# Kernel tuning notes

Hardware: AMD Instinct MI355X
Metric: run time of the kernel (lower is better)

Reference implementation:

```python
import jax, jax.numpy as jnp
import numpy as np

N_NODES = 20000
N_EDGES = 320000
D_IN = 256
D_HID = 256
D_OUT = 128
N_LAYERS = 5
BN_EPS = 1e-5
W_SCALE = 1.0 / np.sqrt(D_HID)


def setup_inputs() -> dict:
    key = jax.random.key(0)
    ks = jax.random.split(key, 16)
    x = jax.random.normal(ks[0], (N_NODES, D_IN), dtype=jnp.float32)
    edge_index = jax.random.randint(ks[1], (2, N_EDGES), 0, N_NODES, dtype=jnp.int32)
    W1 = jax.random.normal(ks[2], (N_LAYERS, D_IN, D_HID), dtype=jnp.float32) * W_SCALE
    b1 = jax.random.normal(ks[3], (N_LAYERS, D_HID), dtype=jnp.float32) * 0.01
    W2a = jax.random.normal(ks[4], (N_LAYERS - 1, D_HID, D_HID), dtype=jnp.float32) * W_SCALE
    b2a = jax.random.normal(ks[5], (N_LAYERS - 1, D_HID), dtype=jnp.float32) * 0.01
    W2_last = jax.random.normal(ks[6], (D_HID, D_OUT), dtype=jnp.float32) * W_SCALE
    b2_last = jax.random.normal(ks[7], (D_OUT,), dtype=jnp.float32) * 0.01
    eps = jnp.zeros((N_LAYERS,), dtype=jnp.float32)
    bn_gamma = jnp.ones((N_LAYERS - 1, D_HID), dtype=jnp.float32)
    bn_beta = jnp.zeros((N_LAYERS - 1, D_HID), dtype=jnp.float32)
    bn_mean = jax.random.normal(ks[8], (N_LAYERS - 1, D_HID), dtype=jnp.float32) * 0.1
    bn_var = jax.random.uniform(ks[9], (N_LAYERS - 1, D_HID), dtype=jnp.float32, minval=0.5, maxval=1.5)
    return {"x": x, "edge_index": edge_index, "W1": W1, "b1": b1, "W2a": W2a,
            "b2a": b2a, "W2_last": W2_last, "b2_last": b2_last, "eps": eps,
            "bn_gamma": bn_gamma, "bn_beta": bn_beta, "bn_mean": bn_mean, "bn_var": bn_var}


def reference(x, edge_index, W1, b1, W2a, b2a, W2_last, b2_last, eps,
              bn_gamma, bn_beta, bn_mean, bn_var):
    src, dst = edge_index[0], edge_index[1]
    n = x.shape[0]

    def gin_conv(h, e, w1, bb1, w2, bb2):
        # scatter-add neighbor sum: agg[v] = sum_{(u->v)} h[u]
        agg = jax.ops.segment_sum(h[src], dst, num_segments=n)  # [N, d]
        z = (1.0 + e) * h + agg
        z = jax.nn.relu(z @ w1 + bb1)
        return z @ w2 + bb2

    h = x
    for i in range(N_LAYERS - 1):
        h = gin_conv(h, eps[i], W1[i], b1[i], W2a[i], b2a[i])
        # BatchNorm1d in eval mode (running stats); dropout inactive at inference
        h = (h - bn_mean[i]) * jax.lax.rsqrt(bn_var[i] + BN_EPS) * bn_gamma[i] + bn_beta[i]
        h = jax.nn.relu(h)
    out = gin_conv(h, eps[N_LAYERS - 1], W1[N_LAYERS - 1], b1[N_LAYERS - 1], W2_last, b2_last)
    return out
```

## Files before the change

kernel.cpp:

```cpp
#include <hip/hip_runtime.h>
#include <stdint.h>

#define NN    20000
#define NE    320000
#define MPAD  20096
#define DD    256
#define DOUT  128
#define CAP   64
#define RS    40
#define SS    1288
#define STS   264
#define SFS   132

typedef unsigned short u16;
typedef __attribute__((ext_vector_type(8))) __bf16 bf16x8;
typedef __attribute__((ext_vector_type(4))) float  f32x4;

__device__ __forceinline__ uint32_t f2b(float f){
  union { float f; uint32_t u; } x; x.f = f;
  uint32_t r = x.u + 0x7FFFu + ((x.u >> 16) & 1u);
  return r >> 16;
}
__device__ __forceinline__ float blo(uint32_t p){ union{uint32_t u;float f;}x; x.u=p<<16;         return x.f; }
__device__ __forceinline__ float bhi(uint32_t p){ union{uint32_t u;float f;}x; x.u=p&0xFFFF0000u; return x.f; }
__device__ __forceinline__ int   fiu(float f){ union{float f;int i;}x; x.f=f; return x.i; }
__device__ __forceinline__ float uif(int i){ union{int i;float f;}x; x.i=i; return x.f; }

#define TB 152
#define XB (MPAD/4)
#define EB ((NE+255)/256)
__global__ __launch_bounds__(256) void prep_all(
    const float* __restrict__ x, const int* __restrict__ src, const int* __restrict__ dst,
    const float* __restrict__ W1, const float* __restrict__ W2a, const float* __restrict__ W2l,
    u16* __restrict__ W1t, u16* __restrict__ W2at, u16* __restrict__ W2lt,
    u16* __restrict__ h0, int* __restrict__ cnt, int* __restrict__ csr)
{
  __shared__ u16 Ts[64][65];
  int b = blockIdx.x, tid = threadIdx.x;
  if (b < TB){
    const float* srcp; u16* dstp; int ldS, k0, n0;
    if (b < 80){
      int layer = b >> 4, sub = b & 15;
      srcp = W1 + layer*65536; dstp = W1t + layer*65536; ldS = 256;
      k0 = (sub >> 2)*64; n0 = (sub & 3)*64;
    } else if (b < 144){
      int bb = b - 80; int layer = bb >> 4, sub = bb & 15;
      srcp = W2a + layer*65536; dstp = W2at + layer*65536; ldS = 256;
      k0 = (sub >> 2)*64; n0 = (sub & 3)*64;
    } else {
      int sub = b - 144;
      srcp = W2l; dstp = W2lt; ldS = 128;
      k0 = (sub >> 1)*64; n0 = (sub & 1)*64;
    }
    int c = tid & 63, r0 = tid >> 6;
    #pragma unroll
    for (int i = 0; i < 16; ++i){
      int r = r0 + i*4;
      Ts[r][c] = (u16)f2b(srcp[(size_t)(k0 + r)*ldS + n0 + c]);
    }
    __syncthreads();
    #pragma unroll
    for (int i = 0; i < 16; ++i){
      int n = r0 + i*4;
      dstp[(size_t)(n0 + n)*256 + k0 + c] = Ts[c][n];
    }
  } else if (b < TB + XB){
    int bb = b - TB;
    int row  = bb*4 + (tid >> 6);
    int lane = tid & 63;
    uint2 o = make_uint2(0u, 0u);
    if (row < NN){
      float4 f = *(const float4*)(x + (size_t)row*DD + lane*4);
      o.x = f2b(f.x) | (f2b(f.y) << 16);
      o.y = f2b(f.z) | (f2b(f.w) << 16);
    }
    *(uint2*)(h0 + (size_t)row*DD + lane*4) = o;
  } else {
    int e = (b - TB - XB)*256 + tid;
    if (e < NE){
      int d = dst[e];
      int slot = atomicAdd(&cnt[d], 1);
      if (slot < CAP) csr[d*CAP + slot] = src[e];
    }
  }
}

__global__ __launch_bounds__(256, 3) void gin_fused(
    const u16* __restrict__ hin, const int* __restrict__ cnt, const int* __restrict__ csr,
    const float* __restrict__ eps_arr, int layer,
    const u16* __restrict__ w1, const float* __restrict__ b1,
    const u16* __restrict__ w2, const float* __restrict__ b2,
    const float* __restrict__ gma, const float* __restrict__ bta,
    const float* __restrict__ mu,  const float* __restrict__ var,
    u16* __restrict__ hout, float* __restrict__ outf, int last)
{
  __shared__ __align__(16) u16 As[8*SS];
  int tid  = threadIdx.x;
  int lane = tid & 63, w = tid >> 6;
  int m0 = blockIdx.x * 32;
  int l15 = lane & 15, l4 = lane >> 4;

  {
    float e = 1.0f + eps_arr[layer];
    int half = lane >> 5, kl = lane & 31;
    int xi = (lane ^ 32) << 2;
    const u16* hrow = hin + kl*8;
    u16* dstL = As + (kl >> 2)*SS + (kl & 3)*8;
    for (int i = 0; i < 8; ++i){
      int row = w*8 + i;
      int v = __builtin_amdgcn_readfirstlane(m0 + row);
      float a0=0.f,a1=0.f,a2=0.f,a3=0.f,a4=0.f,a5=0.f,a6=0.f,a7=0.f;
      if (v < NN){
        uint4 ov = *(const uint4*)(hrow + (size_t)v*DD);
        int deg = cnt[v]; deg = deg > CAP ? CAP : deg;
        const int* lst = csr + (size_t)v*CAP;
        for (int base = 0; base < deg; base += 16){
          int4 q[4];
          #pragma unroll
          for (int c = 0; c < 4; ++c) q[c] = *(const int4*)(lst + base + 4*c);
          int idv[8];
          #pragma unroll
          for (int c = 0; c < 4; ++c){
            idv[2*c]   = half ? q[c].y : q[c].x;
            idv[2*c+1] = half ? q[c].w : q[c].z;
          }
          uint4 rv[8];
          #pragma unroll
          for (int c = 0; c < 8; ++c){
            int g = (base + 2*c + half < deg) ? idv[c] : v;
            rv[c] = *(const uint4*)(hrow + (size_t)g*DD);
          }
          #pragma unroll
          for (int c = 0; c < 8; ++c){
            if (base + 2*c + half < deg){
              a0 += blo(rv[c].x); a1 += bhi(rv[c].x);
              a2 += blo(rv[c].y); a3 += bhi(rv[c].y);
              a4 += blo(rv[c].z); a5 += bhi(rv[c].z);
              a6 += blo(rv[c].w); a7 += bhi(rv[c].w);
            }
          }
        }
        float eh = half ? 0.0f : e;
        a0 += eh*blo(ov.x); a1 += eh*bhi(ov.x);
        a2 += eh*blo(ov.y); a3 += eh*bhi(ov.y);
        a4 += eh*blo(ov.z); a5 += eh*bhi(ov.z);
        a6 += eh*blo(ov.w); a7 += eh*bhi(ov.w);
      }
      a0 += uif(__builtin_amdgcn_ds_bpermute(xi, fiu(a0)));
      a1 += uif(__builtin_amdgcn_ds_bpermute(xi, fiu(a1)));
      a2 += uif(__builtin_amdgcn_ds_bpermute(xi, fiu(a2)));
      a3 += uif(__builtin_amdgcn_ds_bpermute(xi, fiu(a3)));
      a4 += uif(__builtin_amdgcn_ds_bpermute(xi, fiu(a4)));
      a5 += uif(__builtin_amdgcn_ds_bpermute(xi, fiu(a5)));
      a6 += uif(__builtin_amdgcn_ds_bpermute(xi, fiu(a6)));
      a7 += uif(__builtin_amdgcn_ds_bpermute(xi, fiu(a7)));
      if (half == 0){
        uint4 o;
        o.x = f2b(a0) | (f2b(a1) << 16);
        o.y = f2b(a2) | (f2b(a3) << 16);
        o.z = f2b(a4) | (f2b(a5) << 16);
        o.w = f2b(a6) | (f2b(a7) << 16);
        *(uint4*)(dstL + row*RS) = o;
      }
    }
  }
  __syncthreads();

  f32x4 acc1[4][2];
  #pragma unroll
  for (int i=0;i<4;++i)
    #pragma unroll
    for (int j=0;j<2;++j){ f32x4 zr={0.f,0.f,0.f,0.f}; acc1[i][j]=zr; }
  {
    int hidb = w*64;
    for (int s = 0; s < 8; ++s){
      bf16x8 af[4], bz[2];
      #pragma unroll
      for (int mi=0;mi<4;++mi)
        af[mi] = *(const bf16x8*)(w1 + (size_t)(hidb + mi*16 + l15)*DD + s*32 + l4*8);
      #pragma unroll
      for (int nj=0;nj<2;++nj)
        bz[nj] = *(const bf16x8*)(As + s*SS + (nj*16 + l15)*RS + l4*8);
      #pragma unroll
      for (int mi=0;mi<4;++mi)
        #pragma unroll
        for (int nj=0;nj<2;++nj)
          acc1[mi][nj] = __builtin_amdgcn_mfma_f32_16x16x32_bf16(af[mi], bz[nj], acc1[mi][nj], 0,0,0);
    }
  }
  __syncthreads();

  {
    int hidb = w*64;
    #pragma unroll
    for (int mi=0;mi<4;++mi){
      float4 bv = *(const float4*)(b1 + hidb + mi*16 + l4*4);
      int s2 = w*2 + (mi >> 1);
      int kp = (mi & 1)*16 + l4*4;
      #pragma unroll
      for (int nj=0;nj<2;++nj){
        int zrow = nj*16 + l15;
        float v0 = acc1[mi][nj][0] + bv.x; v0 = v0 > 0.f ? v0 : 0.f;
        float v1 = acc1[mi][nj][1] + bv.y; v1 = v1 > 0.f ? v1 : 0.f;
        float v2 = acc1[mi][nj][2] + bv.z; v2 = v2 > 0.f ? v2 : 0.f;
        float v3 = acc1[mi][nj][3] + bv.w; v3 = v3 > 0.f ? v3 : 0.f;
        uint2 pk;
        pk.x = f2b(v0) | (f2b(v1) << 16);
        pk.y = f2b(v2) | (f2b(v3) << 16);
        *(uint2*)(As + s2*SS + zrow*RS + kp) = pk;
      }
    }
  }
  __syncthreads();

  if (!last){
    f32x4 acc2[2][4];
    #pragma unroll
    for (int i=0;i<2;++i)
      #pragma unroll
      for (int j=0;j<4;++j){ f32x4 zr={0.f,0.f,0.f,0.f}; acc2[i][j]=zr; }
    int cb = w*64;
    for (int s = 0; s < 8; ++s){
      bf16x8 at[2], bw[4];
      #pragma unroll
      for (int i=0;i<2;++i)
        at[i] = *(const bf16x8*)(As + s*SS + (i*16 + l15)*RS + l4*8);
      #pragma unroll
      for (int j=0;j<4;++j)
        bw[j] = *(const bf16x8*)(w2 + (size_t)(cb + j*16 + l15)*DD + s*32 + l4*8);
      #pragma unroll
      for (int i=0;i<2;++i)
        #pragma unroll
        for (int j=0;j<4;++j)
          acc2[i][j] = __builtin_amdgcn_mfma_f32_16x16x32_bf16(at[i], bw[j], acc2[i][j], 0,0,0);
    }
    __syncthreads();
    u16* St = As;
    #pragma unroll
    for (int j=0;j<4;++j){
      int col = cb + j*16 + l15;
      float sc = rsqrtf(var[col] + 1e-5f) * gma[col];
      float sh = (b2[col] - mu[col]) * sc + bta[col];
      #pragma unroll
      for (int i=0;i<2;++i){
        #pragma unroll
        for (int r=0;r<4;++r){
          int row = i*16 + l4*4 + r;
          float vv = acc2[i][j][r]*sc + sh;
          vv = vv > 0.f ? vv : 0.f;
          St[row*STS + col] = (u16)f2b(vv);
        }
      }
    }
    __syncthreads();
    #pragma unroll
    for (int it = 0; it < 4; ++it){
      int idx = it*256 + tid;
      int row = idx >> 5, c = idx & 31;
      *(uint4*)(hout + (size_t)(m0 + row)*DD + c*8) = *(const uint4*)(St + row*STS + c*8);
    }
  } else {
    f32x4 acc2[2][2];
    #pragma unroll
    for (int i=0;i<2;++i)
      #pragma unroll
      for (int j=0;j<2;++j){ f32x4 zr={0.f,0.f,0.f,0.f}; acc2[i][j]=zr; }
    int cbk = w*32;
    for (int s = 0; s < 8; ++s){
      bf16x8 at[2], bw[2];
      #pragma unroll
      for (int i=0;i<2;++i)
        at[i] = *(const bf16x8*)(As + s*SS + (i*16 + l15)*RS + l4*8);
      #pragma unroll
      for (int j=0;j<2;++j)
        bw[j] = *(const bf16x8*)(w2 + (size_t)(cbk + j*16 + l15)*DD + s*32 + l4*8);
      #pragma unroll
      for (int i=0;i<2;++i)
        #pragma unroll
        for (int j=0;j<2;++j)
          acc2[i][j] = __builtin_amdgcn_mfma_f32_16x16x32_bf16(at[i], bw[j], acc2[i][j], 0,0,0);
    }
    __syncthreads();
    float* Sf = (float*)As;
    #pragma unroll
    for (int j=0;j<2;++j){
      int col = cbk + j*16 + l15;
      float sh = b2[col];
      #pragma unroll
      for (int i=0;i<2;++i){
        #pragma unroll
        for (int r=0;r<4;++r){
          int row = i*16 + l4*4 + r;
          Sf[row*SFS + col] = acc2[i][j][r] + sh;
        }
      }
    }
    __syncthreads();
    #pragma unroll
    for (int it = 0; it < 4; ++it){
      int idx = it*256 + tid;
      int row = idx >> 5, c = idx & 31;
      if (m0 + row < NN)
        *(uint4*)(outf + (size_t)(m0 + row)*DOUT + c*4) = *(const uint4*)(Sf + row*SFS + c*4);
    }
  }
}

extern "C" void kernel_launch(void* const* d_in, const int* in_sizes, int n_in,
                              void* d_out, int out_size, void* d_ws, size_t ws_size,
                              hipStream_t stream)
{
  const float* x     = (const float*)d_in[0];
  const int*   ei    = (const int*)  d_in[1];
  const float* W1    = (const float*)d_in[2];
  const float* b1    = (const float*)d_in[3];
  const float* W2a   = (const float*)d_in[4];
  const float* b2a   = (const float*)d_in[5];
  const float* W2l   = (const float*)d_in[6];
  const float* b2l   = (const float*)d_in[7];
  const float* eps   = (const float*)d_in[8];
  const float* gma   = (const float*)d_in[9];
  const float* bta   = (const float*)d_in[10];
  const float* mu    = (const float*)d_in[11];
  const float* var   = (const float*)d_in[12];
  float* out = (float*)d_out;

  char* ws = (char*)d_ws;
  size_t off = 0;
  auto alloc = [&](size_t bytes)->void*{
    void* p = ws + off; off += (bytes + 255) & ~(size_t)255; return p;
  };
  u16* h0   = (u16*)alloc((size_t)MPAD*DD*2);
  u16* h1   = (u16*)alloc((size_t)MPAD*DD*2);
  int* cnt  = (int*)alloc((size_t)NN*4);
  int* csr  = (int*)alloc((size_t)NN*CAP*4 + 64);
  u16* W1t  = (u16*)alloc((size_t)5*65536*2);
  u16* W2at = (u16*)alloc((size_t)4*65536*2);
  u16* W2lt = (u16*)alloc((size_t)32768*2);

  const int* srcA = ei;
  const int* dstA = ei + NE;

  hipMemsetAsync(cnt, 0, (size_t)NN*4, stream);
  prep_all<<<TB + XB + EB, 256, 0, stream>>>(x, srcA, dstA, W1, W2a, W2l,
                                             W1t, W2at, W2lt, h0, cnt, csr);

  u16* hbuf[2] = { h0, h1 };
  for (int L = 0; L < 5; ++L){
    const u16* hin = hbuf[L & 1];
    u16*       ho  = hbuf[1 - (L & 1)];
    if (L < 4){
      gin_fused<<<MPAD/32, 256, 0, stream>>>(hin, cnt, csr, eps, L,
          W1t + (size_t)L*65536, b1 + L*256,
          W2at + (size_t)L*65536, b2a + L*256,
          gma + L*256, bta + L*256, mu + L*256, var + L*256,
          ho, nullptr, 0);
    } else {
      gin_fused<<<MPAD/32, 256, 0, stream>>>(hin, cnt, csr, eps, L,
          W1t + (size_t)L*65536, b1 + L*256,
          W2lt, b2l,
          nullptr, nullptr, nullptr, nullptr,
          nullptr, out, 1);
    }
  }
}
```

Baseline: 329.0 us.

## Split neighbor gather into a separate high-occupancy kernel before the MLP GEMM

Unfuses the per-layer kernel into a gather kernel (one wave per node, launch bounds allowing 8 blocks per CU) that writes the aggregated z to global memory, followed by a GEMM kernel that loads z into LDS. The goal is to give the latency-bound random gather more occupancy than the register-heavy fused GEMM kernel permits. The cost is an extra round trip of z through global memory and twice as many launches per layer. The grid is now NN/32, which divides evenly, so the padded rows are no longer processed.

```diff
diff --git a/kernel.cpp b/kernel.cpp
--- a/kernel.cpp
+++ b/kernel.cpp
@@ -74,7 +74,8 @@
       o.x = f2b(f.x) | (f2b(f.y) << 16);
       o.y = f2b(f.z) | (f2b(f.w) << 16);
     }
-    *(uint2*)(h0 + (size_t)row*DD + lane*4) = o;
+    if (row < MPAD)
+      *(uint2*)(h0 + (size_t)row*DD + lane*4) = o;
   } else {
     int e = (b - TB - XB)*256 + tid;
     if (e < NE){
@@ -85,9 +86,73 @@
   }
 }
 
-__global__ __launch_bounds__(256, 3) void gin_fused(
+__global__ __launch_bounds__(256, 8) void gather_z(
     const u16* __restrict__ hin, const int* __restrict__ cnt, const int* __restrict__ csr,
-    const float* __restrict__ eps_arr, int layer,
+    const float* __restrict__ eps_arr, int layer, u16* __restrict__ z)
+{
+  int lane = threadIdx.x & 63;
+  int v = __builtin_amdgcn_readfirstlane(blockIdx.x*4 + (threadIdx.x >> 6));
+  if (v >= NN) return;
+  float e = 1.0f + eps_arr[layer];
+  int half = lane >> 5, kl = lane & 31;
+  int xi = (lane ^ 32) << 2;
+  const u16* hrow = hin + kl*8;
+
+  float a0=0.f,a1=0.f,a2=0.f,a3=0.f,a4=0.f,a5=0.f,a6=0.f,a7=0.f;
+  uint4 ov = *(const uint4*)(hrow + (size_t)v*DD);
+  int deg = cnt[v]; deg = deg > CAP ? CAP : deg;
+  const int* lst = csr + (size_t)v*CAP;
+  for (int base = 0; base < deg; base += 16){
+    int4 q[4];
+    #pragma unroll
+    for (int c = 0; c < 4; ++c) q[c] = *(const int4*)(lst + base + 4*c);
+    int idv[8];
+    #pragma unroll
+    for (int c = 0; c < 4; ++c){
+      idv[2*c]   = half ? q[c].y : q[c].x;
+      idv[2*c+1] = half ? q[c].w : q[c].z;
+    }
+    uint4 rv[8];
+    #pragma unroll
+    for (int c = 0; c < 8; ++c){
+      int g = (base + 2*c + half < deg) ? idv[c] : v;
+      rv[c] = *(const uint4*)(hrow + (size_t)g*DD);
+    }
+    #pragma unroll
+    for (int c = 0; c < 8; ++c){
+      if (base + 2*c + half < deg){
+        a0 += blo(rv[c].x); a1 += bhi(rv[c].x);
+        a2 += blo(rv[c].y); a3 += bhi(rv[c].y);
+        a4 += blo(rv[c].z); a5 += bhi(rv[c].z);
+        a6 += blo(rv[c].w); a7 += bhi(rv[c].w);
+      }
+    }
+  }
+  float eh = half ? 0.0f : e;
+  a0 += eh*blo(ov.x); a1 += eh*bhi(ov.x);
+  a2 += eh*blo(ov.y); a3 += eh*bhi(ov.y);
+  a4 += eh*blo(ov.z); a5 += eh*bhi(ov.z);
+  a6 += eh*blo(ov.w); a7 += eh*bhi(ov.w);
+  a0 += uif(__builtin_amdgcn_ds_bpermute(xi, fiu(a0)));
+  a1 += uif(__builtin_amdgcn_ds_bpermute(xi, fiu(a1)));
+  a2 += uif(__builtin_amdgcn_ds_bpermute(xi, fiu(a2)));
+  a3 += uif(__builtin_amdgcn_ds_bpermute(xi, fiu(a3)));
+  a4 += uif(__builtin_amdgcn_ds_bpermute(xi, fiu(a4)));
+  a5 += uif(__builtin_amdgcn_ds_bpermute(xi, fiu(a5)));
+  a6 += uif(__builtin_amdgcn_ds_bpermute(xi, fiu(a6)));
+  a7 += uif(__builtin_amdgcn_ds_bpermute(xi, fiu(a7)));
+  if (half == 0){
+    uint4 o;
+    o.x = f2b(a0) | (f2b(a1) << 16);
+    o.y = f2b(a2) | (f2b(a3) << 16);
+    o.z = f2b(a4) | (f2b(a5) << 16);
+    o.w = f2b(a6) | (f2b(a7) << 16);
+    *(uint4*)(z + (size_t)v*DD + kl*8) = o;
+  }
+}
+
+__global__ __launch_bounds__(256, 3) void gin_mm(
+    const u16* __restrict__ zin,
     const u16* __restrict__ w1, const float* __restrict__ b1,
     const u16* __restrict__ w2, const float* __restrict__ b2,
     const float* __restrict__ gma, const float* __restrict__ bta,
@@ -100,69 +165,12 @@
   int m0 = blockIdx.x * 32;
   int l15 = lane & 15, l4 = lane >> 4;
 
-  {
-    float e = 1.0f + eps_arr[layer];
-    int half = lane >> 5, kl = lane & 31;
-    int xi = (lane ^ 32) << 2;
-    const u16* hrow = hin + kl*8;
-    u16* dstL = As + (kl >> 2)*SS + (kl & 3)*8;
-    for (int i = 0; i < 8; ++i){
-      int row = w*8 + i;
-      int v = __builtin_amdgcn_readfirstlane(m0 + row);
-      float a0=0.f,a1=0.f,a2=0.f,a3=0.f,a4=0.f,a5=0.f,a6=0.f,a7=0.f;
-      if (v < NN){
-        uint4 ov = *(const uint4*)(hrow + (size_t)v*DD);
-        int deg = cnt[v]; deg = deg > CAP ? CAP : deg;
-        const int* lst = csr + (size_t)v*CAP;
-        for (int base = 0; base < deg; base += 16){
-          int4 q[4];
-          #pragma unroll
-          for (int c = 0; c < 4; ++c) q[c] = *(const int4*)(lst + base + 4*c);
-          int idv[8];
-          #pragma unroll
-          for (int c = 0; c < 4; ++c){
-            idv[2*c]   = half ? q[c].y : q[c].x;
-            idv[2*c+1] = half ? q[c].w : q[c].z;
-          }
-          uint4 rv[8];
-          #pragma unroll
-          for (int c = 0; c < 8; ++c){
-            int g = (base + 2*c + half < deg) ? idv[c] : v;
-            rv[c] = *(const uint4*)(hrow + (size_t)g*DD);
-          }
-          #pragma unroll
-          for (int c = 0; c < 8; ++c){
-            if (base + 2*c + half < deg){
-              a0 += blo(rv[c].x); a1 += bhi(rv[c].x);
-              a2 += blo(rv[c].y); a3 += bhi(rv[c].y);
-              a4 += blo(rv[c].z); a5 += bhi(rv[c].z);
-              a6 += blo(rv[c].w); a7 += bhi(rv[c].w);
-            }
-          }
-        }
-        float eh = half ? 0.0f : e;
-        a0 += eh*blo(ov.x); a1 += eh*bhi(ov.x);
-        a2 += eh*blo(ov.y); a3 += eh*bhi(ov.y);
-        a4 += eh*blo(ov.z); a5 += eh*bhi(ov.z);
-        a6 += eh*blo(ov.w); a7 += eh*bhi(ov.w);
-      }
-      a0 += uif(__builtin_amdgcn_ds_bpermute(xi, fiu(a0)));
-      a1 += uif(__builtin_amdgcn_ds_bpermute(xi, fiu(a1)));
-      a2 += uif(__builtin_amdgcn_ds_bpermute(xi, fiu(a2)));
-      a3 += uif(__builtin_amdgcn_ds_bpermute(xi, fiu(a3)));
-      a4 += uif(__builtin_amdgcn_ds_bpermute(xi, fiu(a4)));
-      a5 += uif(__builtin_amdgcn_ds_bpermute(xi, fiu(a5)));
-      a6 += uif(__builtin_amdgcn_ds_bpermute(xi, fiu(a6)));
-      a7 += uif(__builtin_amdgcn_ds_bpermute(xi, fiu(a7)));
-      if (half == 0){
-        uint4 o;
-        o.x = f2b(a0) | (f2b(a1) << 16);
-        o.y = f2b(a2) | (f2b(a3) << 16);
-        o.z = f2b(a4) | (f2b(a5) << 16);
-        o.w = f2b(a6) | (f2b(a7) << 16);
-        *(uint4*)(dstL + row*RS) = o;
-      }
-    }
+  #pragma unroll
+  for (int it = 0; it < 4; ++it){
+    int idx = it*256 + tid;
+    int row = idx >> 5, kl = idx & 31;
+    uint4 zv = *(const uint4*)(zin + (size_t)(m0 + row)*DD + kl*8);
+    *(uint4*)(As + (kl >> 2)*SS + row*RS + (kl & 3)*8) = zv;
   }
   __syncthreads();
 
@@ -330,8 +338,8 @@
   auto alloc = [&](size_t bytes)->void*{
     void* p = ws + off; off += (bytes + 255) & ~(size_t)255; return p;
   };
-  u16* h0   = (u16*)alloc((size_t)MPAD*DD*2);
-  u16* h1   = (u16*)alloc((size_t)MPAD*DD*2);
+  u16* h    = (u16*)alloc((size_t)MPAD*DD*2);
+  u16* z    = (u16*)alloc((size_t)MPAD*DD*2);
   int* cnt  = (int*)alloc((size_t)NN*4);
   int* csr  = (int*)alloc((size_t)NN*CAP*4 + 64);
   u16* W1t  = (u16*)alloc((size_t)5*65536*2);
@@ -343,21 +351,19 @@
 
   hipMemsetAsync(cnt, 0, (size_t)NN*4, stream);
   prep_all<<<TB + XB + EB, 256, 0, stream>>>(x, srcA, dstA, W1, W2a, W2l,
-                                             W1t, W2at, W2lt, h0, cnt, csr);
-
-  u16* hbuf[2] = { h0, h1 };
+                                             W1t, W2at, W2lt, h, cnt, csr);
+
   for (int L = 0; L < 5; ++L){
-    const u16* hin = hbuf[L & 1];
-    u16*       ho  = hbuf[1 - (L & 1)];
+    gather_z<<<NN/4, 256, 0, stream>>>(h, cnt, csr, eps, L, z);
     if (L < 4){
-      gin_fused<<<MPAD/32, 256, 0, stream>>>(hin, cnt, csr, eps, L,
+      gin_mm<<<NN/32, 256, 0, stream>>>(z,
           W1t + (size_t)L*65536, b1 + L*256,
           W2at + (size_t)L*65536, b2a + L*256,
           gma + L*256, bta + L*256, mu + L*256, var + L*256,
-          ho, nullptr, 0);
+          h, nullptr, 0);
     } else {
-      gin_fused<<<MPAD/32, 256, 0, stream>>>(hin, cnt, csr, eps, L,
-          W1t + (size_t)L*65536, b1 + L*256,
+      gin_mm<<<NN/32, 256, 0, stream>>>(z,
+          W1t + (size_t)4*65536, b1 + 4*256,
           W2lt, b2l,
           nullptr, nullptr, nullptr, nullptr,
           nullptr, out, 1);
```

New measurement: 361.1 us. 9.7% more time.

## Store node features as per-row int8 with scales to shrink neighbor gather traffic

Applied to the files above, without the earlier changes.

Intermediate node features are stored as int8 with a per-row float scale instead of bf16, halving the bytes read in the random neighbor gather, which dominates each layer. The gather is reworked so 16-lane groups each handle one neighbor per step and are reduced with two cross-lane permutes. The layer epilogue quantizes its output rows, and the grid shrinks to 625 blocks, dropping padded rows. The exchange is added quantization error on the input features and on every hidden layer.

```diff
diff --git a/kernel.cpp b/kernel.cpp
--- a/kernel.cpp
+++ b/kernel.cpp
@@ -4,6 +4,7 @@
 #define NN    20000
 #define NE    320000
 #define MPAD  20096
+#define NBLK  625
 #define DD    256
 #define DOUT  128
 #define CAP   64
@@ -13,6 +14,7 @@
 #define SFS   132
 
 typedef unsigned short u16;
+typedef unsigned char  u8;
 typedef __attribute__((ext_vector_type(8))) __bf16 bf16x8;
 typedef __attribute__((ext_vector_type(4))) float  f32x4;
 
@@ -26,6 +28,13 @@
 __device__ __forceinline__ int   fiu(float f){ union{float f;int i;}x; x.f=f; return x.i; }
 __device__ __forceinline__ float uif(int i){ union{int i;float f;}x; x.i=i; return x.f; }
 
+__device__ __forceinline__ void acc4(float* a, uint32_t dw, float s){
+  a[0] += s * (float)(int)(int8_t)(dw);
+  a[1] += s * (float)(int)(int8_t)(dw >> 8);
+  a[2] += s * (float)(int)(int8_t)(dw >> 16);
+  a[3] += s * (float)(int)(int8_t)(dw >> 24);
+}
+
 #define TB 152
 #define XB (MPAD/4)
 #define EB ((NE+255)/256)
@@ -33,7 +42,7 @@
     const float* __restrict__ x, const int* __restrict__ src, const int* __restrict__ dst,
     const float* __restrict__ W1, const float* __restrict__ W2a, const float* __restrict__ W2l,
     u16* __restrict__ W1t, u16* __restrict__ W2at, u16* __restrict__ W2lt,
-    u16* __restrict__ h0, int* __restrict__ cnt, int* __restrict__ csr)
+    u8* __restrict__ hq0, float* __restrict__ hs0, int* __restrict__ cnt, int* __restrict__ csr)
 {
   __shared__ u16 Ts[64][65];
   int b = blockIdx.x, tid = threadIdx.x;
@@ -68,13 +77,21 @@
     int bb = b - TB;
     int row  = bb*4 + (tid >> 6);
     int lane = tid & 63;
-    uint2 o = make_uint2(0u, 0u);
-    if (row < NN){
-      float4 f = *(const float4*)(x + (size_t)row*DD + lane*4);
-      o.x = f2b(f.x) | (f2b(f.y) << 16);
-      o.y = f2b(f.z) | (f2b(f.w) << 16);
-    }
-    *(uint2*)(h0 + (size_t)row*DD + lane*4) = o;
+    float4 f = make_float4(0.f,0.f,0.f,0.f);
+    if (row < NN) f = *(const float4*)(x + (size_t)row*DD + lane*4);
+    float mx = fmaxf(fmaxf(fabsf(f.x), fabsf(f.y)), fmaxf(fabsf(f.z), fabsf(f.w)));
+    #pragma unroll
+    for (int m = 1; m < 64; m <<= 1) mx = fmaxf(mx, __shfl_xor(mx, m, 64));
+    float inv = mx > 0.f ? 127.0f/mx : 0.f;
+    uint32_t pk = 0;
+    pk |= (uint32_t)(u8)(int8_t)__float2int_rn(f.x*inv);
+    pk |= (uint32_t)(u8)(int8_t)__float2int_rn(f.y*inv) << 8;
+    pk |= (uint32_t)(u8)(int8_t)__float2int_rn(f.z*inv) << 16;
+    pk |= (uint32_t)(u8)(int8_t)__float2int_rn(f.w*inv) << 24;
+    if (row < MPAD){
+      *(uint32_t*)(hq0 + (size_t)row*DD + lane*4) = pk;
+      if (lane == 0) hs0[row] = mx * (1.0f/127.0f);
+    }
   } else {
     int e = (b - TB - XB)*256 + tid;
     if (e < NE){
@@ -86,13 +103,15 @@
 }
 
 __global__ __launch_bounds__(256, 3) void gin_fused(
-    const u16* __restrict__ hin, const int* __restrict__ cnt, const int* __restrict__ csr,
+    const u8* __restrict__ hq, const float* __restrict__ hs,
+    const int* __restrict__ cnt, const int* __restrict__ csr,
     const float* __restrict__ eps_arr, int layer,
     const u16* __restrict__ w1, const float* __restrict__ b1,
     const u16* __restrict__ w2, const float* __restrict__ b2,
     const float* __restrict__ gma, const float* __restrict__ bta,
     const float* __restrict__ mu,  const float* __restrict__ var,
-    u16* __restrict__ hout, float* __restrict__ outf, int last)
+    u8* __restrict__ hqo, float* __restrict__ hso,
+    float* __restrict__ outf, int last)
 {
   __shared__ __align__(16) u16 As[8*SS];
   int tid  = threadIdx.x;
@@ -102,65 +121,66 @@
 
   {
     float e = 1.0f + eps_arr[layer];
-    int half = lane >> 5, kl = lane & 31;
-    int xi = (lane ^ 32) << 2;
-    const u16* hrow = hin + kl*8;
-    u16* dstL = As + (kl >> 2)*SS + (kl & 3)*8;
+    int q2 = lane >> 4, kl = lane & 15;
+    int x16 = (lane ^ 16) << 2;
+    int x32 = (lane ^ 32) << 2;
+    const u8* hrow = hq + kl*16;
     for (int i = 0; i < 8; ++i){
       int row = w*8 + i;
       int v = __builtin_amdgcn_readfirstlane(m0 + row);
-      float a0=0.f,a1=0.f,a2=0.f,a3=0.f,a4=0.f,a5=0.f,a6=0.f,a7=0.f;
-      if (v < NN){
+      float a[16];
+      #pragma unroll
+      for (int j = 0; j < 16; ++j) a[j] = 0.f;
+      int deg = cnt[v]; deg = deg > CAP ? CAP : deg;
+      const int* lst = csr + (size_t)v*CAP;
+      for (int base = 0; base < deg; base += 16){
+        int4 qv[4];
+        #pragma unroll
+        for (int c = 0; c < 4; ++c) qv[c] = *(const int4*)(lst + base + 4*c);
+        uint4 rv[4]; float sv[4];
+        #pragma unroll
+        for (int c = 0; c < 4; ++c){
+          int slot = base + 4*c + q2;
+          int eidx = q2 == 0 ? qv[c].x : q2 == 1 ? qv[c].y : q2 == 2 ? qv[c].z : qv[c].w;
+          int g = slot < deg ? eidx : v;
+          rv[c] = *(const uint4*)(hrow + (size_t)g*DD);
+          float s = hs[g];
+          sv[c] = slot < deg ? s : 0.f;
+        }
+        #pragma unroll
+        for (int c = 0; c < 4; ++c){
+          acc4(a +  0, rv[c].x, sv[c]);
+          acc4(a +  4, rv[c].y, sv[c]);
+          acc4(a +  8, rv[c].z, sv[c]);
+          acc4(a + 12, rv[c].w, sv[c]);
+        }
+      }
+      {
         uint4 ov = *(const uint4*)(hrow + (size_t)v*DD);
-        int deg = cnt[v]; deg = deg > CAP ? CAP : deg;
-        const int* lst = csr + (size_t)v*CAP;
-        for (int base = 0; base < deg; base += 16){
-          int4 q[4];
-          #pragma unroll
-          for (int c = 0; c < 4; ++c) q[c] = *(const int4*)(lst + base + 4*c);
-          int idv[8];
-          #pragma unroll
-          for (int c = 0; c < 4; ++c){
-            idv[2*c]   = half ? q[c].y : q[c].x;
-            idv[2*c+1] = half ? q[c].w : q[c].z;
-          }
-          uint4 rv[8];
-          #pragma unroll
-          for (int c = 0; c < 8; ++c){
-            int g = (base + 2*c + half < deg) ? idv[c] : v;
-            rv[c] = *(const uint4*)(hrow + (size_t)g*DD);
-          }
-          #pragma unroll
-          for (int c = 0; c < 8; ++c){
-            if (base + 2*c + half < deg){
-              a0 += blo(rv[c].x); a1 += bhi(rv[c].x);
-              a2 += blo(rv[c].y); a3 += bhi(rv[c].y);
-              a4 += blo(rv[c].z); a5 += bhi(rv[c].z);
-              a6 += blo(rv[c].w); a7 += bhi(rv[c].w);
-            }
-          }
-        }
-        float eh = half ? 0.0f : e;
-        a0 += eh*blo(ov.x); a1 += eh*bhi(ov.x);
-        a2 += eh*blo(ov.y); a3 += eh*bhi(ov.y);
-        a4 += eh*blo(ov.z); a5 += eh*bhi(ov.z);
-        a6 += eh*blo(ov.w); a7 += eh*bhi(ov.w);
-      }
-      a0 += uif(__builtin_amdgcn_ds_bpermute(xi, fiu(a0)));
-      a1 += uif(__builtin_amdgcn_ds_bpermute(xi, fiu(a1)));
-      a2 += uif(__builtin_amdgcn_ds_bpermute(xi, fiu(a2)));
-      a3 += uif(__builtin_amdgcn_ds_bpermute(xi, fiu(a3)));
-      a4 += uif(__builtin_amdgcn_ds_bpermute(xi, fiu(a4)));
-      a5 += uif(__builtin_amdgcn_ds_bpermute(xi, fiu(a5)));
-      a6 += uif(__builtin_amdgcn_ds_bpermute(xi, fiu(a6)));
-      a7 += uif(__builtin_amdgcn_ds_bpermute(xi, fiu(a7)));
-      if (half == 0){
-        uint4 o;
-        o.x = f2b(a0) | (f2b(a1) << 16);
-        o.y = f2b(a2) | (f2b(a3) << 16);
-        o.z = f2b(a4) | (f2b(a5) << 16);
-        o.w = f2b(a6) | (f2b(a7) << 16);
-        *(uint4*)(dstL + row*RS) = o;
+        float se = (q2 == 0) ? e * hs[v] : 0.f;
+        acc4(a +  0, ov.x, se);
+        acc4(a +  4, ov.y, se);
+        acc4(a +  8, ov.z, se);
+        acc4(a + 12, ov.w, se);
+      }
+      #pragma unroll
+      for (int j = 0; j < 16; ++j){
+        a[j] += uif(__builtin_amdgcn_ds_bpermute(x16, fiu(a[j])));
+        a[j] += uif(__builtin_amdgcn_ds_bpermute(x32, fiu(a[j])));
+      }
+      if (q2 == 0){
+        uint4 o1, o2;
+        o1.x = f2b(a[0])  | (f2b(a[1])  << 16);
+        o1.y = f2b(a[2])  | (f2b(a[3])  << 16);
+        o1.z = f2b(a[4])  | (f2b(a[5])  << 16);
+        o1.w = f2b(a[6])  | (f2b(a[7])  << 16);
+        o2.x = f2b(a[8])  | (f2b(a[9])  << 16);
+        o2.y = f2b(a[10]) | (f2b(a[11]) << 16);
+        o2.z = f2b(a[12]) | (f2b(a[13]) << 16);
+        o2.w = f2b(a[14]) | (f2b(a[15]) << 16);
+        u16* dstL = As + (kl >> 1)*SS + row*RS + (kl & 1)*16;
+        *(uint4*)(dstL)     = o1;
+        *(uint4*)(dstL + 8) = o2;
       }
     }
   }
@@ -257,7 +277,24 @@
     for (int it = 0; it < 4; ++it){
       int idx = it*256 + tid;
       int row = idx >> 5, c = idx & 31;
-      *(uint4*)(hout + (size_t)(m0 + row)*DD + c*8) = *(const uint4*)(St + row*STS + c*8);
+      uint4 pk = *(const uint4*)(St + row*STS + c*8);
+      float f0 = blo(pk.x), f1 = bhi(pk.x), f2 = blo(pk.y), f3 = bhi(pk.y);
+      float f4 = blo(pk.z), f5 = bhi(pk.z), f6 = blo(pk.w), f7 = bhi(pk.w);
+      float mx = fmaxf(fmaxf(fmaxf(f0,f1), fmaxf(f2,f3)), fmaxf(fmaxf(f4,f5), fmaxf(f6,f7)));
+      #pragma unroll
+      for (int m = 1; m < 32; m <<= 1) mx = fmaxf(mx, __shfl_xor(mx, m, 64));
+      float inv = mx > 0.f ? 127.0f/mx : 0.f;
+      uint32_t b0 = 0, b1v = 0;
+      b0  |= (uint32_t)(u8)(int8_t)__float2int_rn(f0*inv);
+      b0  |= (uint32_t)(u8)(int8_t)__float2int_rn(f1*inv) << 8;
+      b0  |= (uint32_t)(u8)(int8_t)__float2int_rn(f2*inv) << 16;
+      b0  |= (uint32_t)(u8)(int8_t)__float2int_rn(f3*inv) << 24;
+      b1v |= (uint32_t)(u8)(int8_t)__float2int_rn(f4*inv);
+      b1v |= (uint32_t)(u8)(int8_t)__float2int_rn(f5*inv) << 8;
+      b1v |= (uint32_t)(u8)(int8_t)__float2int_rn(f6*inv) << 16;
+      b1v |= (uint32_t)(u8)(int8_t)__float2int_rn(f7*inv) << 24;
+      *(uint2*)(hqo + (size_t)(m0 + row)*DD + c*8) = make_uint2(b0, b1v);
+      if (c == 0) hso[m0 + row] = mx * (1.0f/127.0f);
     }
   } else {
     f32x4 acc2[2][2];
@@ -300,8 +337,7 @@
     for (int it = 0; it < 4; ++it){
       int idx = it*256 + tid;
       int row = idx >> 5, c = idx & 31;
-      if (m0 + row < NN)
-        *(uint4*)(outf + (size_t)(m0 + row)*DOUT + c*4) = *(const uint4*)(Sf + row*SFS + c*4);
+      *(uint4*)(outf + (size_t)(m0 + row)*DOUT + c*4) = *(const uint4*)(Sf + row*SFS + c*4);
     }
   }
 }
@@ -330,37 +366,42 @@
   auto alloc = [&](size_t bytes)->void*{
     void* p = ws + off; off += (bytes + 255) & ~(size_t)255; return p;
   };
-  u16* h0   = (u16*)alloc((size_t)MPAD*DD*2);
-  u16* h1   = (u16*)alloc((size_t)MPAD*DD*2);
-  int* cnt  = (int*)alloc((size_t)NN*4);
-  int* csr  = (int*)alloc((size_t)NN*CAP*4 + 64);
-  u16* W1t  = (u16*)alloc((size_t)5*65536*2);
-  u16* W2at = (u16*)alloc((size_t)4*65536*2);
-  u16* W2lt = (u16*)alloc((size_t)32768*2);
+  u8*    hq0 = (u8*)   alloc((size_t)MPAD*DD);
+  u8*    hq1 = (u8*)   alloc((size_t)MPAD*DD);
+  float* hs0 = (float*)alloc((size_t)MPAD*4);
+  float* hs1 = (float*)alloc((size_t)MPAD*4);
+  int*   cnt = (int*)  alloc((size_t)NN*4);
+  int*   csr = (int*)  alloc((size_t)NN*CAP*4 + 64);
+  u16*  W1t  = (u16*)  alloc((size_t)5*65536*2);
+  u16*  W2at = (u16*)  alloc((size_t)4*65536*2);
+  u16*  W2lt = (u16*)  alloc((size_t)32768*2);
 
   const int* srcA = ei;
   const int* dstA = ei + NE;
 
   hipMemsetAsync(cnt, 0, (size_t)NN*4, stream);
   prep_all<<<TB + XB + EB, 256, 0, stream>>>(x, srcA, dstA, W1, W2a, W2l,
-                                             W1t, W2at, W2lt, h0, cnt, csr);
-
-  u16* hbuf[2] = { h0, h1 };
+                                             W1t, W2at, W2lt, hq0, hs0, cnt, csr);
+
+  u8*    hq[2] = { hq0, hq1 };
+  float* hsv[2] = { hs0, hs1 };
   for (int L = 0; L < 5; ++L){
-    const u16* hin = hbuf[L & 1];
-    u16*       ho  = hbuf[1 - (L & 1)];
+    const u8*    hin = hq[L & 1];
+    const float* hsi = hsv[L & 1];
+    u8*    ho  = hq[1 - (L & 1)];
+    float* hso = hsv[1 - (L & 1)];
     if (L < 4){
-      gin_fused<<<MPAD/32, 256, 0, stream>>>(hin, cnt, csr, eps, L,
+      gin_fused<<<NBLK, 256, 0, stream>>>(hin, hsi, cnt, csr, eps, L,
           W1t + (size_t)L*65536, b1 + L*256,
           W2at + (size_t)L*65536, b2a + L*256,
           gma + L*256, bta + L*256, mu + L*256, var + L*256,
-          ho, nullptr, 0);
+          ho, hso, nullptr, 0);
     } else {
-      gin_fused<<<MPAD/32, 256, 0, stream>>>(hin, cnt, csr, eps, L,
-          W1t + (size_t)L*65536, b1 + L*256,
+      gin_fused<<<NBLK, 256, 0, stream>>>(hin, hsi, cnt, csr, eps, L,
+          W1t + (size_t)4*65536, b1 + 4*256,
           W2lt, b2l,
           nullptr, nullptr, nullptr, nullptr,
-          nullptr, out, 1);
+          nullptr, nullptr, out, 1);
     }
   }
 }
```

Measured after the change: 352.2 us. 1.07x slower.

## Merge five per-layer launches into one persistent kernel with grid barriers

Applied to the files above, without the earlier changes.

Replaces the five per-layer gin_fused launches with a single gin_all kernel that loops over layers and synchronises all 628 blocks through an atomic-counter grid barrier between layers. The aim is to remove kernel launch gaps and tail effects between layers. It relies on all 628 blocks being co-resident (256 CUs at 3 blocks per CU allows it) and adds spin-wait barrier cost plus a memset of the counter. A bounds guard on h0 writes in prep is also added.

```diff
diff --git a/kernel.cpp b/kernel.cpp
--- a/kernel.cpp
+++ b/kernel.cpp
@@ -4,6 +4,7 @@
 #define NN    20000
 #define NE    320000
 #define MPAD  20096
+#define NBLK  628
 #define DD    256
 #define DOUT  128
 #define CAP   64
@@ -25,6 +26,17 @@
 __device__ __forceinline__ float bhi(uint32_t p){ union{uint32_t u;float f;}x; x.u=p&0xFFFF0000u; return x.f; }
 __device__ __forceinline__ int   fiu(float f){ union{float f;int i;}x; x.f=f; return x.i; }
 __device__ __forceinline__ float uif(int i){ union{int i;float f;}x; x.i=i; return x.f; }
+
+__device__ __forceinline__ void grid_barrier(int* bar, int target){
+  __syncthreads();
+  if (threadIdx.x == 0){
+    __threadfence();
+    __hip_atomic_fetch_add(bar, 1, __ATOMIC_ACQ_REL, __HIP_MEMORY_SCOPE_AGENT);
+    while (__hip_atomic_load(bar, __ATOMIC_ACQUIRE, __HIP_MEMORY_SCOPE_AGENT) < target)
+      __builtin_amdgcn_s_sleep(8);
+  }
+  __syncthreads();
+}
 
 #define TB 152
 #define XB (MPAD/4)
@@ -74,7 +86,8 @@
       o.x = f2b(f.x) | (f2b(f.y) << 16);
       o.y = f2b(f.z) | (f2b(f.w) << 16);
     }
-    *(uint2*)(h0 + (size_t)row*DD + lane*4) = o;
+    if (row < MPAD)
+      *(uint2*)(h0 + (size_t)row*DD + lane*4) = o;
   } else {
     int e = (b - TB - XB)*256 + tid;
     if (e < NE){
@@ -85,14 +98,16 @@
   }
 }
 
-__global__ __launch_bounds__(256, 3) void gin_fused(
-    const u16* __restrict__ hin, const int* __restrict__ cnt, const int* __restrict__ csr,
-    const float* __restrict__ eps_arr, int layer,
-    const u16* __restrict__ w1, const float* __restrict__ b1,
-    const u16* __restrict__ w2, const float* __restrict__ b2,
+__global__ __launch_bounds__(256, 3) void gin_all(
+    u16* __restrict__ h0, u16* __restrict__ h1,
+    const int* __restrict__ cnt, const int* __restrict__ csr,
+    const float* __restrict__ eps_arr,
+    const u16* __restrict__ W1t, const float* __restrict__ b1,
+    const u16* __restrict__ W2at, const float* __restrict__ b2a,
+    const u16* __restrict__ W2lt, const float* __restrict__ b2l,
     const float* __restrict__ gma, const float* __restrict__ bta,
     const float* __restrict__ mu,  const float* __restrict__ var,
-    u16* __restrict__ hout, float* __restrict__ outf, int last)
+    float* __restrict__ outf, int* __restrict__ bar)
 {
   __shared__ __align__(16) u16 As[8*SS];
   int tid  = threadIdx.x;
@@ -100,209 +115,226 @@
   int m0 = blockIdx.x * 32;
   int l15 = lane & 15, l4 = lane >> 4;
 
-  {
-    float e = 1.0f + eps_arr[layer];
-    int half = lane >> 5, kl = lane & 31;
-    int xi = (lane ^ 32) << 2;
-    const u16* hrow = hin + kl*8;
-    u16* dstL = As + (kl >> 2)*SS + (kl & 3)*8;
-    for (int i = 0; i < 8; ++i){
-      int row = w*8 + i;
-      int v = __builtin_amdgcn_readfirstlane(m0 + row);
-      float a0=0.f,a1=0.f,a2=0.f,a3=0.f,a4=0.f,a5=0.f,a6=0.f,a7=0.f;
-      if (v < NN){
-        uint4 ov = *(const uint4*)(hrow + (size_t)v*DD);
-        int deg = cnt[v]; deg = deg > CAP ? CAP : deg;
-        const int* lst = csr + (size_t)v*CAP;
-        for (int base = 0; base < deg; base += 16){
-          int4 q[4];
-          #pragma unroll
-          for (int c = 0; c < 4; ++c) q[c] = *(const int4*)(lst + base + 4*c);
-          int idv[8];
-          #pragma unroll
-          for (int c = 0; c < 4; ++c){
-            idv[2*c]   = half ? q[c].y : q[c].x;
-            idv[2*c+1] = half ? q[c].w : q[c].z;
-          }
-          uint4 rv[8];
-          #pragma unroll
-          for (int c = 0; c < 8; ++c){
-            int g = (base + 2*c + half < deg) ? idv[c] : v;
-            rv[c] = *(const uint4*)(hrow + (size_t)g*DD);
-          }
-          #pragma unroll
-          for (int c = 0; c < 8; ++c){
-            if (base + 2*c + half < deg){
-              a0 += blo(rv[c].x); a1 += bhi(rv[c].x);
-              a2 += blo(rv[c].y); a3 += bhi(rv[c].y);
-              a4 += blo(rv[c].z); a5 += bhi(rv[c].z);
-              a6 += blo(rv[c].w); a7 += bhi(rv[c].w);
+  for (int L = 0; L < 5; ++L){
+    const u16* hin  = (L & 1) ? h1 : h0;
+    u16*       hout = (L & 1) ? h0 : h1;
+    int last = (L == 4);
+    const u16*  w1  = W1t + (size_t)L*65536;
+    const float* b1p = b1 + L*256;
+    const u16*  w2  = last ? W2lt : (W2at + (size_t)L*65536);
+    const float* b2p = last ? b2l : (b2a + L*256);
+    const float* gmaL = gma + L*256;
+    const float* btaL = bta + L*256;
+    const float* muL  = mu  + L*256;
+    const float* varL = var + L*256;
+
+    {
+      float e = 1.0f + eps_arr[L];
+      int half = lane >> 5, kl = lane & 31;
+      int xi = (lane ^ 32) << 2;
+      const u16* hrow = hin + kl*8;
+      u16* dstL = As + (kl >> 2)*SS + (kl & 3)*8;
+      for (int i = 0; i < 8; ++i){
+        int row = w*8 + i;
+        int v = __builtin_amdgcn_readfirstlane(m0 + row);
+        float a0=0.f,a1=0.f,a2=0.f,a3=0.f,a4=0.f,a5=0.f,a6=0.f,a7=0.f;
+        if (v < NN){
+          uint4 ov = *(const uint4*)(hrow + (size_t)v*DD);
+          int deg = cnt[v]; deg = deg > CAP ? CAP : deg;
+          const int* lst = csr + (size_t)v*CAP;
+          for (int base = 0; base < deg; base += 16){
+            int4 q[4];
+            #pragma unroll
+            for (int c = 0; c < 4; ++c) q[c] = *(const int4*)(lst + base + 4*c);
+            int idv[8];
+            #pragma unroll
+            for (int c = 0; c < 4; ++c){
+              idv[2*c]   = half ? q[c].y : q[c].x;
+              idv[2*c+1] = half ? q[c].w : q[c].z;
+            }
+            uint4 rv[8];
+            #pragma unroll
+            for (int c = 0; c < 8; ++c){
+              int g = (base + 2*c + half < deg) ? idv[c] : v;
+              rv[c] = *(const uint4*)(hrow + (size_t)g*DD);
+            }
+            #pragma unroll
+            for (int c = 0; c < 8; ++c){
+              if (base + 2*c + half < deg){
+                a0 += blo(rv[c].x); a1 += bhi(rv[c].x);
+                a2 += blo(rv[c].y); a3 += bhi(rv[c].y);
+                a4 += blo(rv[c].z); a5 += bhi(rv[c].z);
+                a6 += blo(rv[c].w); a7 += bhi(rv[c].w);
+              }
             }
           }
-        }
-        float eh = half ? 0.0f : e;
-        a0 += eh*blo(ov.x); a1 += eh*bhi(ov.x);
-        a2 += eh*blo(ov.y); a3 += eh*bhi(ov.y);
-        a4 += eh*blo(ov.z); a5 += eh*bhi(ov.z);
-        a6 += eh*blo(ov.w); a7 += eh*bhi(ov.w);
-      }
-      a0 += uif(__builtin_amdgcn_ds_bpermute(xi, fiu(a0)));
-      a1 += uif(__builtin_amdgcn_ds_bpermute(xi, fiu(a1)));
-      a2 += uif(__builtin_amdgcn_ds_bpermute(xi, fiu(a2)));
-      a3 += uif(__builtin_amdgcn_ds_bpermute(xi, fiu(a3)));
-      a4 += uif(__builtin_amdgcn_ds_bpermute(xi, fiu(a4)));
-      a5 += uif(__builtin_amdgcn_ds_bpermute(xi, fiu(a5)));
-      a6 += uif(__builtin_amdgcn_ds_bpermute(xi, fiu(a6)));
-      a7 += uif(__builtin_amdgcn_ds_bpermute(xi, fiu(a7)));
-      if (half == 0){
-        uint4 o;
-        o.x = f2b(a0) | (f2b(a1) << 16);
-        o.y = f2b(a2) | (f2b(a3) << 16);
-        o.z = f2b(a4) | (f2b(a5) << 16);
-        o.w = f2b(a6) | (f2b(a7) << 16);
-        *(uint4*)(dstL + row*RS) = o;
-      }
-    }
-  }
-  __syncthreads();
-
-  f32x4 acc1[4][2];
-  #pragma unroll
-  for (int i=0;i<4;++i)
+          float eh = half ? 0.0f : e;
+          a0 += eh*blo(ov.x); a1 += eh*bhi(ov.x);
+          a2 += eh*blo(ov.y); a3 += eh*bhi(ov.y);
+          a4 += eh*blo(ov.z); a5 += eh*bhi(ov.z);
+          a6 += eh*blo(ov.w); a7 += eh*bhi(ov.w);
+        }
+        a0 += uif(__builtin_amdgcn_ds_bpermute(xi, fiu(a0)));
+        a1 += uif(__builtin_amdgcn_ds_bpermute(xi, fiu(a1)));
+        a2 += uif(__builtin_amdgcn_ds_bpermute(xi, fiu(a2)));
+        a3 += uif(__builtin_amdgcn_ds_bpermute(xi, fiu(a3)));
+        a4 += uif(__builtin_amdgcn_ds_bpermute(xi, fiu(a4)));
+        a5 += uif(__builtin_amdgcn_ds_bpermute(xi, fiu(a5)));
+        a6 += uif(__builtin_amdgcn_ds_bpermute(xi, fiu(a6)));
+        a7 += uif(__builtin_amdgcn_ds_bpermute(xi, fiu(a7)));
+        if (half == 0){
+          uint4 o;
+          o.x = f2b(a0) | (f2b(a1) << 16);
+          o.y = f2b(a2) | (f2b(a3) << 16);
+          o.z = f2b(a4) | (f2b(a5) << 16);
+          o.w = f2b(a6) | (f2b(a7) << 16);
+          *(uint4*)(dstL + row*RS) = o;
+        }
+      }
+    }
+    __syncthreads();
+
+    f32x4 acc1[4][2];
     #pragma unroll
-    for (int j=0;j<2;++j){ f32x4 zr={0.f,0.f,0.f,0.f}; acc1[i][j]=zr; }
-  {
-    int hidb = w*64;
-    for (int s = 0; s < 8; ++s){
-      bf16x8 af[4], bz[2];
-      #pragma unroll
-      for (int mi=0;mi<4;++mi)
-        af[mi] = *(const bf16x8*)(w1 + (size_t)(hidb + mi*16 + l15)*DD + s*32 + l4*8);
-      #pragma unroll
-      for (int nj=0;nj<2;++nj)
-        bz[nj] = *(const bf16x8*)(As + s*SS + (nj*16 + l15)*RS + l4*8);
-      #pragma unroll
-      for (int mi=0;mi<4;++mi)
+    for (int i=0;i<4;++i)
+      #pragma unroll
+      for (int j=0;j<2;++j){ f32x4 zr={0.f,0.f,0.f,0.f}; acc1[i][j]=zr; }
+    {
+      int hidb = w*64;
+      for (int s = 0; s < 8; ++s){
+        bf16x8 af[4], bz[2];
+        #pragma unroll
+        for (int mi=0;mi<4;++mi)
+          af[mi] = *(const bf16x8*)(w1 + (size_t)(hidb + mi*16 + l15)*DD + s*32 + l4*8);
         #pragma unroll
         for (int nj=0;nj<2;++nj)
-          acc1[mi][nj] = __builtin_amdgcn_mfma_f32_16x16x32_bf16(af[mi], bz[nj], acc1[mi][nj], 0,0,0);
-    }
-  }
-  __syncthreads();
-
-  {
-    int hidb = w*64;
-    #pragma unroll
-    for (int mi=0;mi<4;++mi){
-      float4 bv = *(const float4*)(b1 + hidb + mi*16 + l4*4);
-      int s2 = w*2 + (mi >> 1);
-      int kp = (mi & 1)*16 + l4*4;
-      #pragma unroll
-      for (int nj=0;nj<2;++nj){
-        int zrow = nj*16 + l15;
-        float v0 = acc1[mi][nj][0] + bv.x; v0 = v0 > 0.f ? v0 : 0.f;
-        float v1 = acc1[mi][nj][1] + bv.y; v1 = v1 > 0.f ? v1 : 0.f;
-        float v2 = acc1[mi][nj][2] + bv.z; v2 = v2 > 0.f ? v2 : 0.f;
-        float v3 = acc1[mi][nj][3] + bv.w; v3 = v3 > 0.f ? v3 : 0.f;
-        uint2 pk;
-        pk.x = f2b(v0) | (f2b(v1) << 16);
-        pk.y = f2b(v2) | (f2b(v3) << 16);
-        *(uint2*)(As + s2*SS + zrow*RS + kp) = pk;
-      }
-    }
-  }
-  __syncthreads();
-
-  if (!last){
-    f32x4 acc2[2][4];
-    #pragma unroll
-    for (int i=0;i<2;++i)
-      #pragma unroll
-      for (int j=0;j<4;++j){ f32x4 zr={0.f,0.f,0.f,0.f}; acc2[i][j]=zr; }
-    int cb = w*64;
-    for (int s = 0; s < 8; ++s){
-      bf16x8 at[2], bw[4];
+          bz[nj] = *(const bf16x8*)(As + s*SS + (nj*16 + l15)*RS + l4*8);
+        #pragma unroll
+        for (int mi=0;mi<4;++mi)
+          #pragma unroll
+          for (int nj=0;nj<2;++nj)
+            acc1[mi][nj] = __builtin_amdgcn_mfma_f32_16x16x32_bf16(af[mi], bz[nj], acc1[mi][nj], 0,0,0);
+      }
+    }
+    __syncthreads();
+
+    {
+      int hidb = w*64;
+      #pragma unroll
+      for (int mi=0;mi<4;++mi){
+        float4 bv = *(const float4*)(b1p + hidb + mi*16 + l4*4);
+        int s2 = w*2 + (mi >> 1);
+        int kp = (mi & 1)*16 + l4*4;
+        #pragma unroll
+        for (int nj=0;nj<2;++nj){
+          int zrow = nj*16 + l15;
+          float v0 = acc1[mi][nj][0] + bv.x; v0 = v0 > 0.f ? v0 : 0.f;
+          float v1 = acc1[mi][nj][1] + bv.y; v1 = v1 > 0.f ? v1 : 0.f;
+          float v2 = acc1[mi][nj][2] + bv.z; v2 = v2 > 0.f ? v2 : 0.f;
+          float v3 = acc1[mi][nj][3] + bv.w; v3 = v3 > 0.f ? v3 : 0.f;
+          uint2 pk;
+          pk.x = f2b(v0) | (f2b(v1) << 16);
+          pk.y = f2b(v2) | (f2b(v3) << 16);
+          *(uint2*)(As + s2*SS + zrow*RS + kp) = pk;
+        }
+      }
+    }
+    __syncthreads();
+
+    if (!last){
+      f32x4 acc2[2][4];
       #pragma unroll
       for (int i=0;i<2;++i)
-        at[i] = *(const bf16x8*)(As + s*SS + (i*16 + l15)*RS + l4*8);
-      #pragma unroll
-      for (int j=0;j<4;++j)
-        bw[j] = *(const bf16x8*)(w2 + (size_t)(cb + j*16 + l15)*DD + s*32 + l4*8);
+        #pragma unroll
+        for (int j=0;j<4;++j){ f32x4 zr={0.f,0.f,0.f,0.f}; acc2[i][j]=zr; }
+      int cb = w*64;
+      for (int s = 0; s < 8; ++s){
+        bf16x8 at[2], bw[4];
+        #pragma unroll
+        for (int i=0;i<2;++i)
+          at[i] = *(const bf16x8*)(As + s*SS + (i*16 + l15)*RS + l4*8);
+        #pragma unroll
+        for (int j=0;j<4;++j)
+          bw[j] = *(const bf16x8*)(w2 + (size_t)(cb + j*16 + l15)*DD + s*32 + l4*8);
+        #pragma unroll
+        for (int i=0;i<2;++i)
+          #pragma unroll
+          for (int j=0;j<4;++j)
+            acc2[i][j] = __builtin_amdgcn_mfma_f32_16x16x32_bf16(at[i], bw[j], acc2[i][j], 0,0,0);
+      }
+      __syncthreads();
+      u16* St = As;
+      #pragma unroll
+      for (int j=0;j<4;++j){
+        int col = cb + j*16 + l15;
+        float sc = rsqrtf(varL[col] + 1e-5f) * gmaL[col];
+        float sh = (b2p[col] - muL[col]) * sc + btaL[col];
+        #pragma unroll
+        for (int i=0;i<2;++i){
+          #pragma unroll
+          for (int r=0;r<4;++r){
+            int row = i*16 + l4*4 + r;
+            float vv = acc2[i][j][r]*sc + sh;
+            vv = vv > 0.f ? vv : 0.f;
+            St[row*STS + col] = (u16)f2b(vv);
+          }
+        }
+      }
+      __syncthreads();
+      #pragma unroll
+      for (int it = 0; it < 4; ++it){
+        int idx = it*256 + tid;
+        int row = idx >> 5, c = idx & 31;
+        *(uint4*)(hout + (size_t)(m0 + row)*DD + c*8) = *(const uint4*)(St + row*STS + c*8);
+      }
+    } else {
+      f32x4 acc2[2][2];
       #pragma unroll
       for (int i=0;i<2;++i)
         #pragma unroll
-        for (int j=0;j<4;++j)
-          acc2[i][j] = __builtin_amdgcn_mfma_f32_16x16x32_bf16(at[i], bw[j], acc2[i][j], 0,0,0);
-    }
-    __syncthreads();
-    u16* St = As;
-    #pragma unroll
-    for (int j=0;j<4;++j){
-      int col = cb + j*16 + l15;
-      float sc = rsqrtf(var[col] + 1e-5f) * gma[col];
-      float sh = (b2[col] - mu[col]) * sc + bta[col];
-      #pragma unroll
-      for (int i=0;i<2;++i){
-        #pragma unroll
-        for (int r=0;r<4;++r){
-          int row = i*16 + l4*4 + r;
-          float vv = acc2[i][j][r]*sc + sh;
-          vv = vv > 0.f ? vv : 0.f;
-          St[row*STS + col] = (u16)f2b(vv);
-        }
-      }
-    }
-    __syncthreads();
-    #pragma unroll
-    for (int it = 0; it < 4; ++it){
-      int idx = it*256 + tid;
-      int row = idx >> 5, c = idx & 31;
-      *(uint4*)(hout + (size_t)(m0 + row)*DD + c*8) = *(const uint4*)(St + row*STS + c*8);
-    }
-  } else {
-    f32x4 acc2[2][2];
-    #pragma unroll
-    for (int i=0;i<2;++i)
-      #pragma unroll
-      for (int j=0;j<2;++j){ f32x4 zr={0.f,0.f,0.f,0.f}; acc2[i][j]=zr; }
-    int cbk = w*32;
-    for (int s = 0; s < 8; ++s){
-      bf16x8 at[2], bw[2];
-      #pragma unroll
-      for (int i=0;i<2;++i)
-        at[i] = *(const bf16x8*)(As + s*SS + (i*16 + l15)*RS + l4*8);
-      #pragma unroll
-      for (int j=0;j<2;++j)
-        bw[j] = *(const bf16x8*)(w2 + (size_t)(cbk + j*16 + l15)*DD + s*32 + l4*8);
-      #pragma unroll
-      for (int i=0;i<2;++i)
+        for (int j=0;j<2;++j){ f32x4 zr={0.f,0.f,0.f,0.f}; acc2[i][j]=zr; }
+      int cbk = w*32;
+      for (int s = 0; s < 8; ++s){
+        bf16x8 at[2], bw[2];
+        #pragma unroll
+        for (int i=0;i<2;++i)
+          at[i] = *(const bf16x8*)(As + s*SS + (i*16 + l15)*RS + l4*8);
         #pragma unroll
         for (int j=0;j<2;++j)
-          acc2[i][j] = __builtin_amdgcn_mfma_f32_16x16x32_bf16(at[i], bw[j], acc2[i][j], 0,0,0);
-    }
-    __syncthreads();
-    float* Sf = (float*)As;
-    #pragma unroll
-    for (int j=0;j<2;++j){
-      int col = cbk + j*16 + l15;
-      float sh = b2[col];
-      #pragma unroll
-      for (int i=0;i<2;++i){
-        #pragma unroll
-        for (int r=0;r<4;++r){
-          int row = i*16 + l4*4 + r;
-          Sf[row*SFS + col] = acc2[i][j][r] + sh;
-        }
-      }
-    }
-    __syncthreads();
-    #pragma unroll
-    for (int it = 0; it < 4; ++it){
-      int idx = it*256 + tid;
-      int row = idx >> 5, c = idx & 31;
-      if (m0 + row < NN)
-        *(uint4*)(outf + (size_t)(m0 + row)*DOUT + c*4) = *(const uint4*)(Sf + row*SFS + c*4);
-    }
+          bw[j] = *(const bf16x8*)(w2 + (size_t)(cbk + j*16 + l15)*DD + s*32 + l4*8);
+        #pragma unroll
+        for (int i=0;i<2;++i)
+          #pragma unroll
+          for (int j=0;j<2;++j)
+            acc2[i][j] = __builtin_amdgcn_mfma_f32_16x16x32_bf16(at[i], bw[j], acc2[i][j], 0,0,0);
+      }
+      __syncthreads();
+      float* Sf = (float*)As;
+      #pragma unroll
+      for (int j=0;j<2;++j){
+        int col = cbk + j*16 + l15;
+        float sh = b2p[col];
+        #pragma unroll
+        for (int i=0;i<2;++i){
+          #pragma unroll
+          for (int r=0;r<4;++r){
+            int row = i*16 + l4*4 + r;
+            Sf[row*SFS + col] = acc2[i][j][r] + sh;
+          }
+        }
+      }
+      __syncthreads();
+      #pragma unroll
+      for (int it = 0; it < 4; ++it){
+        int idx = it*256 + tid;
+        int row = idx >> 5, c = idx & 31;
+        if (m0 + row < NN)
+          *(uint4*)(outf + (size_t)(m0 + row)*DOUT + c*4) = *(const uint4*)(Sf + row*SFS + c*4);
+      }
+    }
+
+    if (L < 4)
+      grid_barrier(bar, NBLK*(L+1));
   }
 }
 
@@ -337,30 +369,17 @@
   u16* W1t  = (u16*)alloc((size_t)5*65536*2);
   u16* W2at = (u16*)alloc((size_t)4*65536*2);
   u16* W2lt = (u16*)alloc((size_t)32768*2);
+  int* bar  = (int*)alloc(256);
 
   const int* srcA = ei;
   const int* dstA = ei + NE;
 
   hipMemsetAsync(cnt, 0, (size_t)NN*4, stream);
+  hipMemsetAsync(bar, 0, 256, stream);
   prep_all<<<TB + XB + EB, 256, 0, stream>>>(x, srcA, dstA, W1, W2a, W2l,
                                              W1t, W2at, W2lt, h0, cnt, csr);
 
-  u16* hbuf[2] = { h0, h1 };
-  for (int L = 0; L < 5; ++L){
-    const u16* hin = hbuf[L & 1];
-    u16*       ho  = hbuf[1 - (L & 1)];
-    if (L < 4){
-      gin_fused<<<MPAD/32, 256, 0, stream>>>(hin, cnt, csr, eps, L,
-          W1t + (size_t)L*65536, b1 + L*256,
-          W2at + (size_t)L*65536, b2a + L*256,
-          gma + L*256, bta + L*256, mu + L*256, var + L*256,
-          ho, nullptr, 0);
-    } else {
-      gin_fused<<<MPAD/32, 256, 0, stream>>>(hin, cnt, csr, eps, L,
-          W1t + (size_t)L*65536, b1 + L*256,
-          W2lt, b2l,
-          nullptr, nullptr, nullptr, nullptr,
-          nullptr, out, 1);
-    }
-  }
-}
+  gin_all<<<NBLK, 256, 0, stream>>>(h0, h1, cnt, csr, eps,
+                                    W1t, b1, W2at, b2a, W2lt, b2l,
+                                    gma, bta, mu, var, out, bar);
+}
```

New measurement: 1.002 ms. +204.5%, slower.
